# Optimization experiments

Hardware: AMD Instinct MI355X
Metric: run time of the kernel (lower is better)

The kernel has to match this reference:

```python
import jax, jax.numpy as jnp
import numpy as np

B, D, H = 4096, 1024, 1024
LN_EPS = 1e-5


def setup_inputs() -> dict:
    key = jax.random.key(0)
    ks = jax.random.split(key, 5)
    return {
        "x": jax.random.normal(ks[0], (B, D), dtype=jnp.float32),
        "prev_h": jax.random.normal(ks[1], (B, H), dtype=jnp.float32),
        "prev_c": jax.random.normal(ks[2], (B, H), dtype=jnp.float32),
        "Wx": jax.random.normal(ks[3], (D, 4 * H), dtype=jnp.float32) * 0.01,
        "Wh": jax.random.normal(ks[4], (H, 4 * H), dtype=jnp.float32) * 0.01,
        "b": jnp.zeros((4 * H,), dtype=jnp.float32),
        "ln_gamma": jnp.ones((4 * H,), dtype=jnp.float32),
        "ln_beta": jnp.zeros((4 * H,), dtype=jnp.float32),
    }


def reference(x, prev_h, prev_c, Wx, Wh, b, ln_gamma, ln_beta):
    # pre-activations: [B, 4H]
    a = x @ Wx + prev_h @ Wh + b
    # LayerNorm over last dim (use_ln=True)
    mu = jnp.mean(a, axis=-1, keepdims=True)
    var = jnp.mean(jnp.square(a - mu), axis=-1, keepdims=True)
    a = (a - mu) * jax.lax.rsqrt(var + LN_EPS) * ln_gamma + ln_beta
    i = jax.nn.sigmoid(a[:, :H])
    f = jax.nn.sigmoid(a[:, H:2 * H])
    o = jax.nn.sigmoid(a[:, 2 * H:3 * H])
    g = jnp.tanh(a[:, 3 * H:])
    next_c = f * prev_c + i * g
    next_h = o * jnp.tanh(next_c)
    # dropout=0.0 -> identity
    return (next_h, next_c)
```

## Files before the change

### kernel.cpp

```cpp
#include <hip/hip_runtime.h>
#include <hip/hip_bf16.h>
#include <stdint.h>

typedef unsigned short u16;
typedef unsigned int u32;
typedef __attribute__((ext_vector_type(8))) short short8;
typedef __attribute__((ext_vector_type(16))) float f32x16;

#define B_DIM 4096
#define D_DIM 1024
#define H_DIM 1024
#define K_DIM 2048
#define N_DIM 4096
#define LN_EPS 1e-5f

__device__ __forceinline__ u16 f2bf(float f) {
    union { float f; uint32_t u; } v; v.f = f;
    uint32_t u = v.u;
    uint32_t r = (u + 0x7FFFu + ((u >> 16) & 1u)) >> 16;
    return (u16)r;
}
__device__ __forceinline__ float bf2f(u16 h) {
    union { uint32_t u; float f; } v; v.u = ((uint32_t)h) << 16;
    return v.f;
}
__device__ __forceinline__ void gld16(const u16* g, u16* l) {
    __builtin_amdgcn_global_load_lds(
        (const __attribute__((address_space(1))) void*)g,
        (__attribute__((address_space(3))) void*)l,
        16, 0, 0);
}
__device__ __forceinline__ float sigm(float x) { return 1.0f / (1.0f + __expf(-x)); }
__device__ __forceinline__ float tanh_fast(float x) { return 1.0f - 2.0f / (__expf(2.0f * x) + 1.0f); }

__global__ __launch_bounds__(256) void prep(const float* __restrict__ x,
                                            const float* __restrict__ h,
                                            const float* __restrict__ Wx,
                                            const float* __restrict__ Wh,
                                            u16* __restrict__ A,
                                            u16* __restrict__ Bt) {
    __shared__ u32 tileT[64 * 32];
    const int t = threadIdx.x;
    if (blockIdx.x < 4096) {
        int id = blockIdx.x * 256 + t;
        int row = id >> 8;
        int col = (id & 255) * 8;
        const float* src = (col < D_DIM) ? (x + (size_t)row * D_DIM + col)
                                         : (h + (size_t)row * H_DIM + (col - D_DIM));
        float4 v0 = ((const float4*)src)[0];
        float4 v1 = ((const float4*)src)[1];
        union { u16 us[8]; uint4 u; } p;
        p.us[0] = f2bf(v0.x); p.us[1] = f2bf(v0.y); p.us[2] = f2bf(v0.z); p.us[3] = f2bf(v0.w);
        p.us[4] = f2bf(v1.x); p.us[5] = f2bf(v1.y); p.us[6] = f2bf(v1.z); p.us[7] = f2bf(v1.w);
        *(uint4*)(A + (size_t)id * 8) = p.u;
    } else {
        const int v = blockIdx.x - 4096;
        const int n0 = (v & 63) * 64;
        const int k0 = (v >> 6) * 64;
        const int n4  = (t & 15) * 4;
        const int kp0 = t >> 4;
#pragma unroll
        for (int p = 0; p < 2; ++p) {
            const int kpair = kp0 + p * 16;
            const int k = k0 + kpair * 2;
            const float* src = (k < D_DIM) ? (Wx + (size_t)k * N_DIM)
                                           : (Wh + (size_t)(k - D_DIM) * N_DIM);
            float4 w0 = *(const float4*)(src + n0 + n4);
            float4 w1 = *(const float4*)(src + N_DIM + n0 + n4);
            const float a0[4] = {w0.x, w0.y, w0.z, w0.w};
            const float a1[4] = {w1.x, w1.y, w1.z, w1.w};
            const int q = kpair >> 2, wd = kpair & 3;
#pragma unroll
            for (int j = 0; j < 4; ++j) {
                const int n = n4 + j;
                const u32 pk = (u32)f2bf(a0[j]) | ((u32)f2bf(a1[j]) << 16);
                tileT[n * 32 + ((q ^ ((n >> 2) & 7)) << 2) + wd] = pk;
            }
        }
        __syncthreads();
        const int n = t >> 2;
        const int qb = (t & 3) * 2;
        const int sw = (n >> 2) & 7;
        uint4 r0 = *(const uint4*)&tileT[n * 32 + ((qb ^ sw) << 2)];
        uint4 r1 = *(const uint4*)&tileT[n * 32 + (((qb + 1) ^ sw) << 2)];
        u16* dst = Bt + (size_t)(n0 + n) * K_DIM + k0 + (t & 3) * 16;
        *(uint4*)dst = r0;
        *(uint4*)(dst + 8) = r1;
    }
}

__global__ __launch_bounds__(512, 2) void gemm_bf16(const u16* __restrict__ A,
                                                    const u16* __restrict__ Bt,
                                                    const float* __restrict__ bias,
                                                    u16* __restrict__ C) {
    __shared__ u16 As[2][2][8192];
    __shared__ u16 Bs[2][2][8192];
    const int tid = threadIdx.x;
    const int wave = tid >> 6, lane = tid & 63;

    const int bid = blockIdx.y * 16 + blockIdx.x;
    const int swz_bid = (bid & 7) * 32 + (bid >> 3);
    const int m0 = (swz_bid >> 4) * 256;
    const int n0 = (swz_bid & 15) * 256;

    const int wm = (wave & 1) * 128;
    const int wn = (wave >> 1) * 64;
    const int lr = lane & 31, half = lane >> 5;

    f32x16 acc[4][2] = {};

    const int srow = wave * 16 + (lane >> 2);
    const int qsrc = (lane & 3) ^ ((lane >> 3) & 3);
    const u16* Asrc = A  + (size_t)(m0 + srow) * K_DIM + qsrc * 8;
    const u16* Bsrc = Bt + (size_t)(n0 + srow) * K_DIM + qsrc * 8;
    const int ldst = wave * 512;

    auto stage = [&](int buf, int tt, int ks) {
        const int ko = (tt & 31) * 64 + ks * 32;
        gld16(Asrc + ko,                       &As[buf][ks][ldst]);
        gld16(Asrc + ko + (size_t)128 * K_DIM, &As[buf][ks][ldst + 4096]);
        gld16(Bsrc + ko,                       &Bs[buf][ks][ldst]);
        gld16(Bsrc + ko + (size_t)128 * K_DIM, &Bs[buf][ks][ldst + 4096]);
    };

    const int sA = (lr >> 1) & 3;
    const int aoff = (wm + lr) * 32;
    const int boff = (wn + lr) * 32;

    short8 af[2][4], bf[2][2];

#define PHASE(BUF, KS, STAGE_STMT)                                                     \
    {                                                                                  \
        _Pragma("unroll")                                                              \
        for (int kk = 0; kk < 2; ++kk) {                                               \
            _Pragma("unroll")                                                          \
            for (int i = 0; i < 4; ++i)                                                \
                af[kk][i] = *(const short8*)(                                          \
                    &As[BUF][KS][aoff + i * 1024 + (((kk * 2 + half) ^ sA) << 3)]);    \
            _Pragma("unroll")                                                          \
            for (int qj = 0; qj < 2; ++qj)                                             \
                bf[kk][qj] = *(const short8*)(                                         \
                    &Bs[BUF][KS][boff + qj * 1024 + (((kk * 2 + half) ^ sA) << 3)]);   \
        }                                                                              \
        STAGE_STMT;                                                                    \
        __builtin_amdgcn_s_setprio(1);                                                 \
        _Pragma("unroll")                                                              \
        for (int kk = 0; kk < 2; ++kk)                                                 \
            _Pragma("unroll")                                                          \
            for (int i = 0; i < 4; ++i)                                                \
                _Pragma("unroll")                                                      \
                for (int qj = 0; qj < 2; ++qj)                                         \
                    acc[i][qj] = __builtin_amdgcn_mfma_f32_32x32x16_bf16(              \
                        af[kk][i], bf[kk][qj], acc[i][qj], 0, 0, 0);                   \
        __builtin_amdgcn_s_setprio(0);                                                 \
        asm volatile("s_waitcnt vmcnt(4)" ::: "memory");                               \
        __builtin_amdgcn_s_barrier();                                                  \
        asm volatile("" ::: "memory");                                                 \
    }

    stage(0, 0, 0);
    stage(0, 0, 1);
    stage(1, 1, 0);
    asm volatile("s_waitcnt vmcnt(8)" ::: "memory");
    __builtin_amdgcn_s_barrier();
    asm volatile("" ::: "memory");

    for (int it = 0; it < 16; ++it) {
        const int t = it * 2;
        PHASE(0, 0, stage(1, t + 1, 1));
        PHASE(0, 1, stage(0, t + 2, 0));
        PHASE(1, 0, stage(0, t + 2, 1));
        PHASE(1, 1, stage(1, t + 3, 0));
    }
#undef PHASE

#pragma unroll
    for (int i = 0; i < 4; ++i) {
#pragma unroll
        for (int j = 0; j < 2; ++j) {
            const int c = n0 + wn + 32 * j + lr;
            const float bb = bias[c];
#pragma unroll
            for (int reg = 0; reg < 16; ++reg) {
                const int row = m0 + wm + 32 * i + (reg & 3) + 8 * (reg >> 2) + 4 * half;
                C[(size_t)row * N_DIM + c] = f2bf(acc[i][j][reg] + bb);
            }
        }
    }
}

__global__ __launch_bounds__(256) void ln_lstm(const u16* __restrict__ aT,
                                               const float* __restrict__ pc,
                                               const float* __restrict__ gamma,
                                               const float* __restrict__ beta,
                                               float* __restrict__ out) {
    const int row = blockIdx.x * 4 + (threadIdx.x >> 6);
    const int lane = threadIdx.x & 63;
    const u16* ar = aT + (size_t)row * N_DIM;
    const int j0 = lane * 16;

    union U4 { uint4 u; u16 us[8]; };
    U4 g8[4][2];
#pragma unroll
    for (int s = 0; s < 4; ++s) {
        g8[s][0].u = *(const uint4*)(ar + s * H_DIM + j0);
        g8[s][1].u = *(const uint4*)(ar + s * H_DIM + j0 + 8);
    }

    float sum = 0.f, ssq = 0.f;
#pragma unroll
    for (int s = 0; s < 4; ++s)
#pragma unroll
        for (int hh = 0; hh < 2; ++hh)
#pragma unroll
            for (int e = 0; e < 8; ++e) {
                float v = bf2f(g8[s][hh].us[e]);
                sum += v; ssq += v * v;
            }
#pragma unroll
    for (int m = 1; m < 64; m <<= 1) {
        sum += __shfl_xor(sum, m, 64);
        ssq += __shfl_xor(ssq, m, 64);
    }
    const float mu = sum * (1.0f / N_DIM);
    const float var = fmaxf(ssq * (1.0f / N_DIM) - mu * mu, 0.0f);
    const float rs = rsqrtf(var + LN_EPS);

#pragma unroll
    for (int r = 0; r < 4; ++r) {
        const int c0 = j0 + r * 4;
        float vv[4][4];
#pragma unroll
        for (int s = 0; s < 4; ++s) {
            float4 gm = *(const float4*)(gamma + s * H_DIM + c0);
            float4 bt = *(const float4*)(beta + s * H_DIM + c0);
            const int hh = r >> 1;
            const int e0 = (r & 1) * 4;
            vv[s][0] = (bf2f(g8[s][hh].us[e0 + 0]) - mu) * rs * gm.x + bt.x;
            vv[s][1] = (bf2f(g8[s][hh].us[e0 + 1]) - mu) * rs * gm.y + bt.y;
            vv[s][2] = (bf2f(g8[s][hh].us[e0 + 2]) - mu) * rs * gm.z + bt.z;
            vv[s][3] = (bf2f(g8[s][hh].us[e0 + 3]) - mu) * rs * gm.w + bt.w;
        }
        float4 c4 = *(const float4*)(pc + (size_t)row * H_DIM + c0);
        float cin[4] = {c4.x, c4.y, c4.z, c4.w};
        float nh[4], nc[4];
#pragma unroll
        for (int e = 0; e < 4; ++e) {
            float ig = sigm(vv[0][e]);
            float fg = sigm(vv[1][e]);
            float og = sigm(vv[2][e]);
            float gg = tanh_fast(vv[3][e]);
            nc[e] = fg * cin[e] + ig * gg;
            nh[e] = og * tanh_fast(nc[e]);
        }
        float4 h4 = {nh[0], nh[1], nh[2], nh[3]};
        float4 c4o = {nc[0], nc[1], nc[2], nc[3]};
        *(float4*)(out + (size_t)row * H_DIM + c0) = h4;
        *(float4*)(out + (size_t)B_DIM * H_DIM + (size_t)row * H_DIM + c0) = c4o;
    }
}

extern "C" void kernel_launch(void* const* d_in, const int* in_sizes, int n_in,
                              void* d_out, int out_size, void* d_ws, size_t ws_size,
                              hipStream_t stream) {
    const float* x  = (const float*)d_in[0];
    const float* ph = (const float*)d_in[1];
    const float* pc = (const float*)d_in[2];
    const float* Wx = (const float*)d_in[3];
    const float* Wh = (const float*)d_in[4];
    const float* b  = (const float*)d_in[5];
    const float* gm = (const float*)d_in[6];
    const float* bt = (const float*)d_in[7];
    float* out = (float*)d_out;

    char* ws = (char*)d_ws;
    u16* Abf = (u16*)ws;
    u16* Btb = (u16*)(ws + (size_t)16 * 1024 * 1024);
    u16* aT  = (u16*)(ws + (size_t)32 * 1024 * 1024);

    prep<<<dim3(4096 + 2048), dim3(256), 0, stream>>>(x, ph, Wx, Wh, Abf, Btb);
    gemm_bf16<<<dim3(16, 16), dim3(512), 0, stream>>>(Abf, Btb, b, aT);
    ln_lstm<<<dim3(1024), dim3(256), 0, stream>>>(aT, pc, gm, bt, out);
}
```

Before: 224.3 us.

## Load GEMM B operand directly from global into registers, bypassing LDS

Drops the shared-memory staging buffer for the B (weight) tile. Each wave now loads its B MFMA fragments straight from global memory into double-buffered registers one phase ahead, while A stays staged through LDS. The goal is to halve LDS footprint and LDS read traffic. In exchange, waves that share a column slice fetch the same B data redundantly, each lane reads 16-byte pieces from widely strided rows, and the compiler's own dependency waits may expose global-memory latency inside the MFMA loop.

```diff
diff --git a/kernel.cpp b/kernel.cpp
--- a/kernel.cpp
+++ b/kernel.cpp
@@ -94,7 +94,6 @@
                                                     const float* __restrict__ bias,
                                                     u16* __restrict__ C) {
     __shared__ u16 As[2][2][8192];
-    __shared__ u16 Bs[2][2][8192];
     const int tid = threadIdx.x;
     const int wave = tid >> 6, lane = tid & 63;
 
@@ -111,38 +110,41 @@
 
     const int srow = wave * 16 + (lane >> 2);
     const int qsrc = (lane & 3) ^ ((lane >> 3) & 3);
-    const u16* Asrc = A  + (size_t)(m0 + srow) * K_DIM + qsrc * 8;
-    const u16* Bsrc = Bt + (size_t)(n0 + srow) * K_DIM + qsrc * 8;
+    const u16* Asrc = A + (size_t)(m0 + srow) * K_DIM + qsrc * 8;
     const int ldst = wave * 512;
 
-    auto stage = [&](int buf, int tt, int ks) {
+    auto stageA = [&](int buf, int tt, int ks) {
         const int ko = (tt & 31) * 64 + ks * 32;
         gld16(Asrc + ko,                       &As[buf][ks][ldst]);
         gld16(Asrc + ko + (size_t)128 * K_DIM, &As[buf][ks][ldst + 4096]);
-        gld16(Bsrc + ko,                       &Bs[buf][ks][ldst]);
-        gld16(Bsrc + ko + (size_t)128 * K_DIM, &Bs[buf][ks][ldst + 4096]);
+    };
+
+    const u16* Bgl = Bt + (size_t)(n0 + wn + lr) * K_DIM + half * 8;
+    auto bfload = [&](short8* dst, int tt, int ks) {
+        const int kb = (tt & 31) * 64 + ks * 32;
+#pragma unroll
+        for (int kk = 0; kk < 2; ++kk)
+#pragma unroll
+            for (int qj = 0; qj < 2; ++qj)
+                dst[kk * 2 + qj] = *(const short8*)(
+                    Bgl + (size_t)(qj * 32) * K_DIM + kb + kk * 16);
     };
 
     const int sA = (lr >> 1) & 3;
     const int aoff = (wm + lr) * 32;
-    const int boff = (wn + lr) * 32;
-
-    short8 af[2][4], bf[2][2];
-
-#define PHASE(BUF, KS, STAGE_STMT)                                                     \
+
+    short8 af[2][4], bfE[4], bfO[4];
+
+#define PHASE(BUF, KS, BFC, BFN, TN, KSN, SBUF, ST, SKS)                               \
     {                                                                                  \
+        bfload(BFN, TN, KSN);                                                          \
+        stageA(SBUF, ST, SKS);                                                         \
         _Pragma("unroll")                                                              \
-        for (int kk = 0; kk < 2; ++kk) {                                               \
+        for (int kk = 0; kk < 2; ++kk)                                                 \
             _Pragma("unroll")                                                          \
             for (int i = 0; i < 4; ++i)                                                \
                 af[kk][i] = *(const short8*)(                                          \
                     &As[BUF][KS][aoff + i * 1024 + (((kk * 2 + half) ^ sA) << 3)]);    \
-            _Pragma("unroll")                                                          \
-            for (int qj = 0; qj < 2; ++qj)                                             \
-                bf[kk][qj] = *(const short8*)(                                         \
-                    &Bs[BUF][KS][boff + qj * 1024 + (((kk * 2 + half) ^ sA) << 3)]);   \
-        }                                                                              \
-        STAGE_STMT;                                                                    \
         __builtin_amdgcn_s_setprio(1);                                                 \
         _Pragma("unroll")                                                              \
         for (int kk = 0; kk < 2; ++kk)                                                 \
@@ -151,26 +153,27 @@
                 _Pragma("unroll")                                                      \
                 for (int qj = 0; qj < 2; ++qj)                                         \
                     acc[i][qj] = __builtin_amdgcn_mfma_f32_32x32x16_bf16(              \
-                        af[kk][i], bf[kk][qj], acc[i][qj], 0, 0, 0);                   \
+                        af[kk][i], BFC[kk * 2 + qj], acc[i][qj], 0, 0, 0);             \
         __builtin_amdgcn_s_setprio(0);                                                 \
-        asm volatile("s_waitcnt vmcnt(4)" ::: "memory");                               \
+        asm volatile("s_waitcnt vmcnt(6)" ::: "memory");                               \
         __builtin_amdgcn_s_barrier();                                                  \
         asm volatile("" ::: "memory");                                                 \
     }
 
-    stage(0, 0, 0);
-    stage(0, 0, 1);
-    stage(1, 1, 0);
-    asm volatile("s_waitcnt vmcnt(8)" ::: "memory");
+    stageA(0, 0, 0);
+    stageA(0, 0, 1);
+    stageA(1, 1, 0);
+    bfload(bfE, 0, 0);
+    asm volatile("s_waitcnt vmcnt(0)" ::: "memory");
     __builtin_amdgcn_s_barrier();
     asm volatile("" ::: "memory");
 
     for (int it = 0; it < 16; ++it) {
         const int t = it * 2;
-        PHASE(0, 0, stage(1, t + 1, 1));
-        PHASE(0, 1, stage(0, t + 2, 0));
-        PHASE(1, 0, stage(0, t + 2, 1));
-        PHASE(1, 1, stage(1, t + 3, 0));
+        PHASE(0, 0, bfE, bfO, t,     1, 1, t + 1, 1);
+        PHASE(0, 1, bfO, bfE, t + 1, 0, 0, t + 2, 0);
+        PHASE(1, 0, bfE, bfO, t + 1, 1, 0, t + 2, 1);
+        PHASE(1, 1, bfO, bfE, t + 2, 0, 1, t + 3, 0);
     }
 #undef PHASE
 
```

Result: slower. 249.5 us (+11.3%).
